# Kernel tuning notes

Measured on AMD Instinct MI355X. Metric: run time of the kernel, lower is better.

## Reference

```python
import jax, jax.numpy as jnp
import numpy as np

B, S, E, R = 128, 16, 512, 1000
_SCALE = np.float32(1.0 / np.sqrt(E))


def setup_inputs() -> dict:
    key = jax.random.key(0)
    ks = jax.random.split(key, 12)
    s = 1.0 / np.sqrt(E)
    u = lambda k, shape: jax.random.uniform(k, shape, jnp.float32, -s, s)
    emb = jax.random.normal(ks[0], (R + 1, E), jnp.float32).at[R].set(0.0)  # padding_idx row = 0
    return {
        "tokens": jax.random.randint(ks[11], (B, S), 0, R),
        "emb": emb,
        "W_ih": u(ks[1], (3 * E, E)), "W_hh": u(ks[2], (3 * E, E)),
        "b_ih": u(ks[3], (3 * E,)), "b_hh": u(ks[4], (3 * E,)),
        "w_fc": u(ks[5], (E,)), "b_fc": u(ks[6], ()),
        "Wq": u(ks[7], (E, E)), "bq": u(ks[8], (E,)),
        "Wk": u(ks[9], (E, E)), "bk": u(ks[10], (E,)),
    }


def _gru_step(x, h, W_ih, W_hh, b_ih, b_hh):
    # torch GRU cell: gates stacked as [r; z; n]
    gi = x @ W_ih.T + b_ih
    gh = h @ W_hh.T + b_hh
    ir, iz, inn = jnp.split(gi, 3, axis=-1)
    hr, hz, hn = jnp.split(gh, 3, axis=-1)
    r = jax.nn.sigmoid(ir + hr)
    z = jax.nn.sigmoid(iz + hz)
    n = jnp.tanh(inn + r * hn)
    return (1.0 - z) * n + z * h


def _attention(x, emb, Wq, bq, Wk, bk):
    # x: [B,1,E]; key = fc_k(cat(relation_emb, x)); scores = q k^T / sqrt(E)
    Bn = x.shape[0]
    rel = jnp.broadcast_to(emb[:R][None], (Bn, R, E))
    all_emb = jnp.concatenate([rel, x], axis=1)        # [B,R+1,E]
    q = x @ Wq.T + bq
    k = all_emb @ Wk.T + bk
    scores = jnp.einsum('bqe,bke->bqk', q, k) * _SCALE  # [B,1,R+1]
    return scores, all_emb


def _entropy(scores):
    lp = jax.nn.log_softmax(scores, axis=-1)
    return -jnp.sum(jnp.exp(lp) * lp, axis=-1)          # [B,1]


def _reduce(x, emb, W_ih, W_hh, b_ih, b_hh, w_fc, b_fc, Wq, bq, Wk, bk):
    Bn, L, Ed = x.shape
    if L > 2:
        # vectorized 2-step GRU over all adjacent pairs (replaces python while loop)
        h1 = _gru_step(x[:, :-1], jnp.zeros_like(x[:, :-1]), W_ih, W_hh, b_ih, b_hh)
        pairs = _gru_step(x[:, 1:], h1, W_ih, W_hh, b_ih, b_hh)   # [B,L-1,E]
        score = jax.nn.sigmoid(pairs @ w_fc + b_fc)               # [B,L-1]
        sel = jnp.argmax(score, axis=-1)                          # [B]
        barange = jnp.arange(Bn)
        pair = pairs[barange, sel][:, None]                       # [B,1,E]
        scores, all_emb = _attention(pair, emb, Wq, bq, Wk, bk)
        loss = _entropy(scores)
        prob = jax.nn.softmax(scores, axis=-1)                    # weightedAverage mask is all-False for seq_len=1
        merged = jnp.einsum('bqk,bke->bqe', prob, all_emb)[:, 0]  # [B,E]
        # output = inputs.detach().clone(); overwrite sel with merged; delete row sel+1
        out = jax.lax.stop_gradient(x).at[barange, sel].set(merged)
        j = jnp.arange(L - 1)[None]
        src = j + (j >= (sel + 1)[:, None])                       # skip zeroed row sel+1
        out = out[barange[:, None], src]                          # [B,L-1,E]
        return out, loss
    else:
        h1 = _gru_step(x[:, 0], jnp.zeros_like(x[:, 0]), W_ih, W_hh, b_ih, b_hh)
        h2 = _gru_step(x[:, 1], h1, W_ih, W_hh, b_ih, b_hh)
        return h2[:, None], jnp.zeros((Bn, 1), x.dtype)


def reference(tokens, emb, W_ih, W_hh, b_ih, b_hh, w_fc, b_fc, Wq, bq, Wk, bk):
    x = emb[tokens]                                               # [B,S,E]
    losses = []
    for _ in range(tokens.shape[1] - 1):
        x, l = _reduce(x, emb, W_ih, W_hh, b_ih, b_hh, w_fc, b_fc, Wq, bq, Wk, bk)
        losses.append(l)
    scores, _ = _attention(x, emb, Wq, bq, Wk, bk)                # x is [B,1,E]
    losses.append(_entropy(scores))
    return scores[:, 0], jnp.concatenate(losses, axis=-1)         # ([B,R+1], [B,S])
```

## Files before the change

### kernel.cpp

```cpp
#include <hip/hip_runtime.h>

#define B 128
#define S 16
#define E 512
#define R 1000
#define K3 1536
#define NW0 1920
#define NWS 256
#define NS (B * (R + 1))
#define SCALE 0.04419417382415922f

static __device__ __forceinline__ float sigm(float x) { return 1.f / (1.f + expf(-x)); }

static __device__ __forceinline__ float brsum(float v, float* sb) {
  int tid = threadIdx.x;
  sb[tid] = v; __syncthreads();
  for (int s = 128; s > 0; s >>= 1) {
    if (tid < s) sb[tid] += sb[tid + s];
    __syncthreads();
  }
  float r = sb[0]; __syncthreads();
  return r;
}
static __device__ __forceinline__ float brmax(float v, float* sb) {
  int tid = threadIdx.x;
  sb[tid] = v; __syncthreads();
  for (int s = 128; s > 0; s >>= 1) {
    if (tid < s) sb[tid] = fmaxf(sb[tid], sb[tid + s]);
    __syncthreads();
  }
  float r = sb[0]; __syncthreads();
  return r;
}
static __device__ __forceinline__ void brsum2(float v1, float v2, float* sb, float* sb2,
                                              float* o1, float* o2) {
  int tid = threadIdx.x;
  sb[tid] = v1; sb2[tid] = v2; __syncthreads();
  for (int s = 128; s > 0; s >>= 1) {
    if (tid < s) { sb[tid] += sb[tid + s]; sb2[tid] += sb2[tid + s]; }
    __syncthreads();
  }
  *o1 = sb[0]; *o2 = sb2[0]; __syncthreads();
}

#define TILE_FMA \
  _Pragma("unroll") \
  for (int k = 0; k < 16; ++k) { \
    float4 a4 = *(const float4*)&As[k][ty * 4]; \
    float4 w4 = *(const float4*)&Ws[k][tx * 4]; \
    acc[0][0] = fmaf(a4.x, w4.x, acc[0][0]); acc[0][1] = fmaf(a4.x, w4.y, acc[0][1]); \
    acc[0][2] = fmaf(a4.x, w4.z, acc[0][2]); acc[0][3] = fmaf(a4.x, w4.w, acc[0][3]); \
    acc[1][0] = fmaf(a4.y, w4.x, acc[1][0]); acc[1][1] = fmaf(a4.y, w4.y, acc[1][1]); \
    acc[1][2] = fmaf(a4.y, w4.z, acc[1][2]); acc[1][3] = fmaf(a4.y, w4.w, acc[1][3]); \
    acc[2][0] = fmaf(a4.z, w4.x, acc[2][0]); acc[2][1] = fmaf(a4.z, w4.y, acc[2][1]); \
    acc[2][2] = fmaf(a4.z, w4.z, acc[2][2]); acc[2][3] = fmaf(a4.z, w4.w, acc[2][3]); \
    acc[3][0] = fmaf(a4.w, w4.x, acc[3][0]); acc[3][1] = fmaf(a4.w, w4.y, acc[3][1]); \
    acc[3][2] = fmaf(a4.w, w4.z, acc[3][2]); acc[3][3] = fmaf(a4.w, w4.w, acc[3][3]); \
  }

#define TILE_FMA32 \
  _Pragma("unroll") \
  for (int k = 0; k < 16; ++k) { \
    float2 a2 = *(const float2*)&As[k][ty * 2]; \
    float4 w4 = *(const float4*)&Ws[k][tx * 4]; \
    acc[0][0] = fmaf(a2.x, w4.x, acc[0][0]); acc[0][1] = fmaf(a2.x, w4.y, acc[0][1]); \
    acc[0][2] = fmaf(a2.x, w4.z, acc[0][2]); acc[0][3] = fmaf(a2.x, w4.w, acc[0][3]); \
    acc[1][0] = fmaf(a2.y, w4.x, acc[1][0]); acc[1][1] = fmaf(a2.y, w4.y, acc[1][1]); \
    acc[1][2] = fmaf(a2.y, w4.z, acc[1][2]); acc[1][3] = fmaf(a2.y, w4.w, acc[1][3]); \
  }

__global__ __launch_bounds__(256) void k_gemm(const float* __restrict__ A, int lda, int M,
                                              const float* __restrict__ W, int N, int K,
                                              const float* __restrict__ bias, float scale,
                                              float* __restrict__ C, int ldc) {
  __shared__ float As[16][64];
  __shared__ float Ws[16][64];
  int tid = threadIdx.x;
  int mBase = blockIdx.y * 64;
  int nBase = blockIdx.x * 64;
  int tx = tid & 15, ty = tid >> 4;
  int li = tid & 63;
  int lk = (tid >> 6) * 4;
  float acc[4][4] = {{0.f,0.f,0.f,0.f},{0.f,0.f,0.f,0.f},{0.f,0.f,0.f,0.f},{0.f,0.f,0.f,0.f}};
  int m = mBase + li;
  const float* Arow = (m < M) ? (A + (size_t)m * lda) : nullptr;
  int n = nBase + li;
  const float* Wrow = (n < N) ? (W + (size_t)n * K) : nullptr;

  float4 av = Arow ? *(const float4*)(Arow + lk) : make_float4(0.f, 0.f, 0.f, 0.f);
  float4 wv = Wrow ? *(const float4*)(Wrow + lk) : make_float4(0.f, 0.f, 0.f, 0.f);

  for (int k0 = 0; k0 < K; k0 += 16) {
    As[lk + 0][li] = av.x; As[lk + 1][li] = av.y;
    As[lk + 2][li] = av.z; As[lk + 3][li] = av.w;
    Ws[lk + 0][li] = wv.x; Ws[lk + 1][li] = wv.y;
    Ws[lk + 2][li] = wv.z; Ws[lk + 3][li] = wv.w;
    __syncthreads();
    if (k0 + 16 < K) {
      av = Arow ? *(const float4*)(Arow + k0 + 16 + lk) : make_float4(0.f, 0.f, 0.f, 0.f);
      wv = Wrow ? *(const float4*)(Wrow + k0 + 16 + lk) : make_float4(0.f, 0.f, 0.f, 0.f);
    }
    TILE_FMA
    __syncthreads();
  }
#pragma unroll
  for (int r = 0; r < 4; ++r) {
    int mm = mBase + ty * 4 + r;
    if (mm >= M) continue;
#pragma unroll
    for (int c = 0; c < 4; ++c) {
      int nn = nBase + tx * 4 + c;
      if (nn >= N) continue;
      float v = acc[r][c] * scale;
      if (bias) v += bias[nn];
      C[(size_t)mm * ldc + nn] = v;
    }
  }
}

__global__ __launch_bounds__(256) void k_gemmD(const float* __restrict__ A, int lda, int M,
                                               const float* __restrict__ W1, int N1,
                                               const float* __restrict__ b1,
                                               float* __restrict__ C1, int ldc1,
                                               const float* __restrict__ W2, int N2,
                                               float* __restrict__ C2, int ldc2, int K) {
  __shared__ float As[16][64];
  __shared__ float Ws[16][64];
  int tid = threadIdx.x;
  int mBase = blockIdx.y * 64;
  int nBase = blockIdx.x * 64;
  int tx = tid & 15, ty = tid >> 4;
  int li = tid & 63;
  int lk = (tid >> 6) * 4;
  float acc[4][4] = {{0.f,0.f,0.f,0.f},{0.f,0.f,0.f,0.f},{0.f,0.f,0.f,0.f},{0.f,0.f,0.f,0.f}};
  int m = mBase + li;
  const float* Arow = (m < M) ? (A + (size_t)m * lda) : nullptr;
  int n = nBase + li;
  const float* Wrow = nullptr;
  if (n < N1) Wrow = W1 + (size_t)n * K;
  else if (n < N1 + N2) Wrow = W2 + (size_t)(n - N1) * K;

  float4 av = Arow ? *(const float4*)(Arow + lk) : make_float4(0.f, 0.f, 0.f, 0.f);
  float4 wv = Wrow ? *(const float4*)(Wrow + lk) : make_float4(0.f, 0.f, 0.f, 0.f);

  for (int k0 = 0; k0 < K; k0 += 16) {
    As[lk + 0][li] = av.x; As[lk + 1][li] = av.y;
    As[lk + 2][li] = av.z; As[lk + 3][li] = av.w;
    Ws[lk + 0][li] = wv.x; Ws[lk + 1][li] = wv.y;
    Ws[lk + 2][li] = wv.z; Ws[lk + 3][li] = wv.w;
    __syncthreads();
    if (k0 + 16 < K) {
      av = Arow ? *(const float4*)(Arow + k0 + 16 + lk) : make_float4(0.f, 0.f, 0.f, 0.f);
      wv = Wrow ? *(const float4*)(Wrow + k0 + 16 + lk) : make_float4(0.f, 0.f, 0.f, 0.f);
    }
    TILE_FMA
    __syncthreads();
  }
#pragma unroll
  for (int r = 0; r < 4; ++r) {
    int mm = mBase + ty * 4 + r;
    if (mm >= M) continue;
#pragma unroll
    for (int c = 0; c < 4; ++c) {
      int nn = nBase + tx * 4 + c;
      if (nn < N1) {
        float v = acc[r][c];
        if (b1) v += b1[nn];
        C1[(size_t)mm * ldc1 + nn] = v;
      } else if (nn < N1 + N2) {
        C2[(size_t)mm * ldc2 + (nn - N1)] = acc[r][c];
      }
    }
  }
}

static __device__ void dev_g64(float (*As)[64], float (*Ws)[64], int tid,
                               int mBase, int nBase,
                               const float* __restrict__ A, int lda, int M,
                               const float* __restrict__ W, int N, int K,
                               const float* __restrict__ bias, float scale,
                               float* __restrict__ C, int ldc) {
  int tx = tid & 15, ty = tid >> 4;
  int li = tid & 63;
  int lk = (tid >> 6) * 4;
  float acc[4][4] = {{0.f,0.f,0.f,0.f},{0.f,0.f,0.f,0.f},{0.f,0.f,0.f,0.f},{0.f,0.f,0.f,0.f}};
  int m = mBase + li;
  const float* Arow = (m < M) ? (A + (size_t)m * lda) : nullptr;
  int n = nBase + li;
  const float* Wrow = (n < N) ? (W + (size_t)n * K) : nullptr;

  float4 av = Arow ? *(const float4*)(Arow + lk) : make_float4(0.f, 0.f, 0.f, 0.f);
  float4 wv = Wrow ? *(const float4*)(Wrow + lk) : make_float4(0.f, 0.f, 0.f, 0.f);

  for (int k0 = 0; k0 < K; k0 += 16) {
    As[lk + 0][li] = av.x; As[lk + 1][li] = av.y;
    As[lk + 2][li] = av.z; As[lk + 3][li] = av.w;
    Ws[lk + 0][li] = wv.x; Ws[lk + 1][li] = wv.y;
    Ws[lk + 2][li] = wv.z; Ws[lk + 3][li] = wv.w;
    __syncthreads();
    if (k0 + 16 < K) {
      av = Arow ? *(const float4*)(Arow + k0 + 16 + lk) : make_float4(0.f, 0.f, 0.f, 0.f);
      wv = Wrow ? *(const float4*)(Wrow + k0 + 16 + lk) : make_float4(0.f, 0.f, 0.f, 0.f);
    }
    TILE_FMA
    __syncthreads();
  }
#pragma unroll
  for (int r = 0; r < 4; ++r) {
    int mm = mBase + ty * 4 + r;
    if (mm >= M) continue;
#pragma unroll
    for (int c = 0; c < 4; ++c) {
      int nn = nBase + tx * 4 + c;
      if (nn >= N) continue;
      float v = acc[r][c] * scale;
      if (bias) v += bias[nn];
      C[(size_t)mm * ldc + nn] = v;
    }
  }
}

static __device__ void dev_tr64(float (*t)[65], int tid, const float* __restrict__ src,
                                int Cc, float* __restrict__ dst, int ldd, int bx, int by) {
  int tx = tid & 15, ty = tid >> 4;
  int rb = by * 64, cb = bx * 64;
#pragma unroll
  for (int i = 0; i < 4; ++i) {
    int r = rb + ty + i * 16;
    float4 v = *(const float4*)(src + (size_t)r * Cc + cb + tx * 4);
    t[ty + i * 16][tx * 4 + 0] = v.x; t[ty + i * 16][tx * 4 + 1] = v.y;
    t[ty + i * 16][tx * 4 + 2] = v.z; t[ty + i * 16][tx * 4 + 3] = v.w;
  }
  __syncthreads();
#pragma unroll
  for (int i = 0; i < 4; ++i) {
    int c = cb + ty + i * 16;
    float4 v;
    v.x = t[tx * 4 + 0][ty + i * 16]; v.y = t[tx * 4 + 1][ty + i * 16];
    v.z = t[tx * 4 + 2][ty + i * 16]; v.w = t[tx * 4 + 3][ty + i * 16];
    *(float4*)(dst + (size_t)c * ldd + rb + tx * 4) = v;
  }
}

__global__ __launch_bounds__(256) void k_prep(const float* __restrict__ Wq,
                                              const float* __restrict__ Wk,
                                              const float* __restrict__ Wih,
                                              float* __restrict__ WqT,
                                              float* __restrict__ WkT,
                                              float* __restrict__ Wbig,
                                              int* __restrict__ pos,
                                              int* __restrict__ wlb,
                                              int* __restrict__ wlL,
                                              int* __restrict__ wlR,
                                              float* __restrict__ outp) {
  __shared__ float t[64][65];
  int blk = blockIdx.x, tid = threadIdx.x;
  if (blk < 64) {
    dev_tr64(t, tid, Wq, E, WqT, E, blk & 7, blk >> 3);
  } else if (blk < 128) {
    int j = blk - 64;
    dev_tr64(t, tid, Wk, E, WkT, E, j & 7, j >> 3);
  } else if (blk < 320) {
    int j = blk - 128;
    dev_tr64(t, tid, Wih, E, Wbig + (size_t)1024 * K3, K3, j & 7, j >> 3);
  } else if (blk < 328) {
    int idx = (blk - 320) * 256 + tid;
    if (idx < B * 16) pos[idx] = idx & 15;
    if (idx < NW0) {
      wlb[idx] = idx / 15;
      int i = idx % 15;
      wlL[idx] = i;
      wlR[idx] = i + 1;
    }
    if (idx < B) outp[NS + idx * 16 + 14] = 0.f;
  } else {
    int idx = (blk - 328) * 256 + tid;
    for (int i = idx; i < 24 * K3; i += 8 * 256) Wbig[(size_t)1000 * K3 + i] = 0.f;
  }
}

__global__ __launch_bounds__(256) void k_setup3(const float* __restrict__ KREL,
                                                const float* __restrict__ WqT,
                                                const float* __restrict__ WkT,
                                                const float* __restrict__ bq,
                                                const float* __restrict__ bk,
                                                float* __restrict__ Gbig,
                                                float* __restrict__ v12,
                                                float* __restrict__ c0s,
                                                float* __restrict__ gb,
                                                const int* __restrict__ tokens,
                                                const float* __restrict__ Wbig,
                                                const float* __restrict__ bih,
                                                const float* __restrict__ bhh,
                                                float* __restrict__ GI,
                                                float* __restrict__ H1P,
                                                float* __restrict__ SCT) {
  __shared__ float As[16][64];
  __shared__ float Ws[16][64];
  int blk = blockIdx.x, tid = threadIdx.x;
  if (blk < 128) {
    dev_g64(As, Ws, tid, (blk >> 3) * 64, (blk & 7) * 64, KREL, E, R, WqT, E, E,
            nullptr, 1.f, Gbig, E);
  } else if (blk < 192) {
    int j = blk - 128;
    dev_g64(As, Ws, tid, (j >> 3) * 64, (j & 7) * 64, WqT, E, E, WkT, E, E,
            nullptr, 1.f, Gbig + (size_t)1000 * E, E);
  } else if (blk < 199) {
    int m = blk - 192;
    if (m < 2) {
      int i = m * 256 + tid;
      const float* wq = WqT + (size_t)i * E;
      const float* wk = WkT + (size_t)i * E;
      float s = 0.f;
      for (int e = 0; e < E; ++e) s += wq[e] * bk[e] + bq[e] * wk[e];
      v12[i] = s;
    } else if (m == 2) {
      float* sb = (float*)As;
      float p = 0.f;
      for (int e = tid; e < E; e += 256) p += bq[e] * bk[e];
      float s = brsum(p, sb);
      if (tid == 0) c0s[0] = s;
    } else {
      int r = (m - 3) * 256 + tid;
      if (r < R) {
        const float* kr = KREL + (size_t)r * E;
        float s = 0.f;
        for (int e = 0; e < E; ++e) s += bq[e] * kr[e];
        gb[r] = s;
      }
    }
  } else if (blk < 199 + B * S) {
    int row = blk - 199;
    int tok = tokens[row];
    const float4* src = (const float4*)(Wbig + (size_t)tok * K3);
    const float4* bv = (const float4*)bih;
    float* girow = GI + (size_t)row * K3;
    float4* dst = (float4*)girow;
    for (int i = tid; i < K3 / 4; i += 256) {
      float4 a = src[i], b = bv[i];
      dst[i] = make_float4(a.x + b.x, a.y + b.y, a.z + b.z, a.w + b.w);
    }
    __syncthreads();
    float* h = H1P + (size_t)row * E;
    for (int e = tid; e < E; e += 256) {
      float r = sigm(girow[e] + bhh[e]);
      float z = sigm(girow[E + e] + bhh[E + e]);
      h[e] = (1.f - z) * tanhf(girow[2 * E + e] + r * bhh[2 * E + e]);
    }
  } else {
    int rb = blk - (199 + B * S);
    for (int m = rb * 16; m < rb * 16 + 16; ++m) {
      float* r = SCT + (size_t)m * K3;
      for (int n = tid; n < 1512; n += 256) r[n] = 0.f;
    }
  }
}

__global__ __launch_bounds__(256) void k_h1c(const int* __restrict__ xdst,
                                             const float* __restrict__ GI,
                                             const float* __restrict__ bhh,
                                             float* __restrict__ H1P) {
  int p = xdst[blockIdx.x], tid = threadIdx.x;
  const float* gi = GI + (size_t)p * K3;
  float* h = H1P + (size_t)p * E;
  for (int e = tid; e < E; e += 256) {
    float r = sigm(gi[e] + bhh[e]);
    float z = sigm(gi[E + e] + bhh[E + e]);
    h[e] = (1.f - z) * tanhf(gi[2 * E + e] + r * bhh[2 * E + e]);
  }
}

__global__ __launch_bounds__(256) void k_ghcs(const int* __restrict__ xdst,
                                              const float* __restrict__ H1P,
                                              const float* __restrict__ Whh,
                                              float* __restrict__ GHCP) {
  __shared__ float As[16][32];
  __shared__ float Ws[16][64];
  __shared__ int sp[32];
  int tid = threadIdx.x;
  int nBase = blockIdx.x * 64;
  int mBase = blockIdx.y * 32;
  int kbeg = blockIdx.z * 256;
  if (tid < 32) sp[tid] = xdst[mBase + tid];
  __syncthreads();
  int tx = tid & 15, ty = tid >> 4;
  int ar = tid & 31, ak = (tid >> 5) * 2;
  int li = tid & 63, lk = (tid >> 6) * 4;
  float acc[2][4] = {{0.f,0.f,0.f,0.f},{0.f,0.f,0.f,0.f}};
  const float* Arow = H1P + (size_t)sp[ar] * E + kbeg;
  const float* Wrow = Whh + (size_t)(nBase + li) * E + kbeg;
  float2 av = *(const float2*)(Arow + ak);
  float4 wv = *(const float4*)(Wrow + lk);
  for (int k0 = 0; k0 < 256; k0 += 16) {
    As[ak + 0][ar] = av.x; As[ak + 1][ar] = av.y;
    Ws[lk + 0][li] = wv.x; Ws[lk + 1][li] = wv.y;
    Ws[lk + 2][li] = wv.z; Ws[lk + 3][li] = wv.w;
    __syncthreads();
    if (k0 + 16 < 256) {
      av = *(const float2*)(Arow + k0 + 16 + ak);
      wv = *(const float4*)(Wrow + k0 + 16 + lk);
    }
    TILE_FMA32
    __syncthreads();
  }
#pragma unroll
  for (int r = 0; r < 2; ++r) {
    size_t crow = (size_t)sp[ty * 2 + r] * K3;
#pragma unroll
    for (int c = 0; c < 4; ++c) {
      int nn = nBase + tx * 4 + c;
      atomicAdd(&GHCP[crow + nn], acc[r][c]);
    }
  }
}

__global__ __launch_bounds__(256) void k_pairc(const int* __restrict__ wlb,
                                               const int* __restrict__ wlL,
                                               const int* __restrict__ wlR,
                                               const float* __restrict__ GI,
                                               const float* __restrict__ GHCP,
                                               const float* __restrict__ H1P,
                                               const float* __restrict__ wfc,
                                               const float* __restrict__ bfc,
                                               float* __restrict__ PAIR,
                                               float* __restrict__ SCR) {
  __shared__ float sb[256];
  int w = blockIdx.x, tid = threadIdx.x;
  int b = wlb[w], ls = wlL[w], rs = wlR[w];
  int lp = b * 16 + ls;
  const float* gr = GI + (size_t)(b * 16 + rs) * K3;
  const float* gh = GHCP + (size_t)lp * K3;
  const float* h = H1P + (size_t)lp * E;
  float* p = PAIR + (size_t)lp * E;
  float part = 0.f;
  for (int e = tid; e < E; e += 256) {
    float r = sigm(gr[e] + gh[e]);
    float z = sigm(gr[E + e] + gh[E + e]);
    float n = tanhf(gr[2 * E + e] + r * gh[2 * E + e]);
    float pv = (1.f - z) * n + z * h[e];
    p[e] = pv;
    part += pv * wfc[e];
  }
  float d = brsum(part, sb);
  if (tid == 0) SCR[b * 16 + ls] = sigm(d + bfc[0]);
}

__global__ __launch_bounds__(256) void k_qscsel(const float* __restrict__ PAIR,
                                                const float* __restrict__ SCR,
                                                const int* __restrict__ pin,
                                                int* __restrict__ pout,
                                                int* __restrict__ wlb,
                                                int* __restrict__ wlL,
                                                int* __restrict__ wlR,
                                                int* __restrict__ xdst,
                                                const float* __restrict__ Gbig,
                                                float* __restrict__ SCT,
                                                float* __restrict__ GI,
                                                const float* __restrict__ bih,
                                                float* __restrict__ GHCP,
                                                const float* __restrict__ bhh,
                                                int P, int finalMode) {
  __shared__ float As[16][32];
  __shared__ float Ws[16][64];
  __shared__ int sxd[32];
  int tid = threadIdx.x;
  int nBase = blockIdx.x * 64;
  int mBase = blockIdx.y * 32;
  int kbeg = blockIdx.z * 256;
  if (tid < 32) {
    int b = mBase + tid;
    if (finalMode) {
      int xr = b * 16 + pin[b * 16];
      sxd[tid] = xr;
      if (blockIdx.x == 0 && blockIdx.z == 0) xdst[b] = xr;
    } else {
      int L = P + 1;
      int lp[16];
      for (int i = 0; i < L; ++i) lp[i] = pin[b * 16 + i];
      float best = -1e30f; int sel = 0;
      for (int i = 0; i < P; ++i) {
        float v = SCR[b * 16 + lp[i]];
        if (v > best) { best = v; sel = i; }
      }
      int r1i = (sel + 2 < L) ? sel + 2 : L - 1;
      int l1 = lp[sel], r1 = lp[r1i];
      int l0 = (sel > 0) ? lp[sel - 1] : l1;
      int r0 = (sel > 0) ? lp[sel] : r1;
      sxd[tid] = b * 16 + l1;
      if (blockIdx.x == 0 && blockIdx.z == 0) {
        wlb[2 * b] = b;     wlL[2 * b] = l0;     wlR[2 * b] = r0;
        wlb[2 * b + 1] = b; wlL[2 * b + 1] = l1; wlR[2 * b + 1] = r1;
        xdst[b] = b * 16 + l1;
        for (int i = 0; i < L - 1; ++i)
          pout[b * 16 + i] = (i <= sel) ? lp[i] : lp[i + 1];
      }
    }
  }
  __syncthreads();
  if (!finalMode && blockIdx.z == 1) {
    if (blockIdx.x < 16) {
#pragma unroll
      for (int r = 0; r < 2; ++r) {
        float* g = GI + (size_t)sxd[blockIdx.x * 2 + r] * K3;
        for (int i = tid; i < K3; i += 256) g[i] = bih[i];
      }
    } else {
#pragma unroll
      for (int r = 0; r < 4; ++r) {
        float* g = GHCP + (size_t)sxd[(blockIdx.x - 16) * 4 + r] * K3;
        for (int i = tid; i < K3; i += 256) g[i] = bhh[i];
      }
    }
  }
  int tx = tid & 15, ty = tid >> 4;
  int ar = tid & 31, ak = (tid >> 5) * 2;
  int li = tid & 63, lk = (tid >> 6) * 4;
  float acc[2][4] = {{0.f,0.f,0.f,0.f},{0.f,0.f,0.f,0.f}};
  const float* Arow = PAIR + (size_t)sxd[ar] * E + kbeg;
  int n = nBase + li;
  const float* Wrow = (n < 1512) ? (Gbig + (size_t)n * E + kbeg) : nullptr;
  float2 av = *(const float2*)(Arow + ak);
  float4 wv = Wrow ? *(const float4*)(Wrow + lk) : make_float4(0.f, 0.f, 0.f, 0.f);
  for (int k0 = 0; k0 < 256; k0 += 16) {
    As[ak + 0][ar] = av.x; As[ak + 1][ar] = av.y;
    Ws[lk + 0][li] = wv.x; Ws[lk + 1][li] = wv.y;
    Ws[lk + 2][li] = wv.z; Ws[lk + 3][li] = wv.w;
    __syncthreads();
    if (k0 + 16 < 256) {
      av = *(const float2*)(Arow + k0 + 16 + ak);
      wv = Wrow ? *(const float4*)(Wrow + k0 + 16 + lk) : make_float4(0.f, 0.f, 0.f, 0.f);
    }
    TILE_FMA32
    __syncthreads();
  }
#pragma unroll
  for (int r = 0; r < 2; ++r) {
    int mm = mBase + ty * 2 + r;
#pragma unroll
    for (int c = 0; c < 4; ++c) {
      int nn = nBase + tx * 4 + c;
      if (nn < 1512) atomicAdd(&SCT[(size_t)mm * K3 + nn], acc[r][c]);
    }
  }
}

__global__ __launch_bounds__(256) void k_sm(float* __restrict__ SCT,
                                            const float* __restrict__ PAIR,
                                            const int* __restrict__ xdst,
                                            const float* __restrict__ v12,
                                            const float* __restrict__ c0s,
                                            float* __restrict__ outp,
                                            float* __restrict__ A2,
                                            const float* __restrict__ gb,
                                            int t, int finalMode) {
  __shared__ float sb[256];
  __shared__ float sb2[256];
  __shared__ float sps[E];
  int b = blockIdx.x, tid = threadIdx.x;
  float* row = SCT + (size_t)b * K3;
  int xr = xdst[b];
  const float* sp = PAIR + (size_t)xr * E;
  for (int i = tid; i < E; i += 256) sps[i] = sp[i];
  __syncthreads();
  float part = 0.f;
  for (int i = tid; i < E; i += 256) part += sps[i] * (row[1000 + i] + v12[i]);
  float last = (brsum(part, sb) + c0s[0]) * SCALE;
  float s[4];
  float ml = last;
#pragma unroll
  for (int q = 0; q < 4; ++q) {
    int j = tid + q * 256;
    s[q] = (j < 1000) ? (row[j] + gb[j]) * SCALE : -1e30f;
    ml = fmaxf(ml, s[q]);
  }
  float mx = brmax(ml, sb);
  float zp = 0.f, s1p = 0.f;
#pragma unroll
  for (int q = 0; q < 4; ++q) {
    int j = tid + q * 256;
    if (j < 1000) { float e = expf(s[q] - mx); zp += e; s1p += e * s[q]; }
  }
  if (tid == 0) { float e = expf(last - mx); zp += e; s1p += e * last; }
  float z, s1;
  brsum2(zp, s1p, sb, sb2, &z, &s1);
  if (tid == 0) outp[NS + b * 16 + t] = mx + logf(z) - s1 / z;
  if (!finalMode) {
    float inv = 1.f / z;
    float* a = A2 + (size_t)b * K3;
#pragma unroll
    for (int q = 0; q < 4; ++q) {
      int j = tid + q * 256;
      if (j < 1000) a[j] = expf(s[q] - mx) * inv;
    }
    if (tid < 24) a[1000 + tid] = 0.f;
    float pr = expf(last - mx) * inv;
    for (int i = tid; i < E; i += 256) a[1024 + i] = pr * sps[i];
    for (int n2 = tid; n2 < 1512; n2 += 256) row[n2] = 0.f;
  } else {
    float* so = outp + (size_t)b * (R + 1);
#pragma unroll
    for (int q = 0; q < 4; ++q) {
      int j = tid + q * 256;
      if (j < 1000) so[j] = s[q];
    }
    if (tid == 0) so[R] = last;
  }
}

__global__ __launch_bounds__(256) void k_giup(const float* __restrict__ A2,
                                              const float* __restrict__ Wbig,
                                              float* __restrict__ GI,
                                              const int* __restrict__ xdst) {
  __shared__ float As[16][32];
  __shared__ float Ws[16][64];
  int tid = threadIdx.x;
  int nBase = blockIdx.x * 64;
  int mBase = blockIdx.y * 32;
  int kbeg = blockIdx.z * 384;
  int kend = kbeg + 384;
  int tx = tid & 15, ty = tid >> 4;
  int ar = tid & 31, ak = (tid >> 5) * 2;
  int li = tid & 63, wr = tid >> 6;
  float acc[2][4] = {{0.f,0.f,0.f,0.f},{0.f,0.f,0.f,0.f}};
  const float* Arow = A2 + (size_t)(mBase + ar) * K3;
  float2 av = *(const float2*)(Arow + kbeg + ak);
  float w0 = Wbig[(size_t)(kbeg + wr * 4 + 0) * K3 + nBase + li];
  float w1 = Wbig[(size_t)(kbeg + wr * 4 + 1) * K3 + nBase + li];
  float w2 = Wbig[(size_t)(kbeg + wr * 4 + 2) * K3 + nBase + li];
  float w3 = Wbig[(size_t)(kbeg + wr * 4 + 3) * K3 + nBase + li];
  for (int k0 = kbeg; k0 < kend; k0 += 16) {
    As[ak + 0][ar] = av.x; As[ak + 1][ar] = av.y;
    Ws[wr * 4 + 0][li] = w0; Ws[wr * 4 + 1][li] = w1;
    Ws[wr * 4 + 2][li] = w2; Ws[wr * 4 + 3][li] = w3;
    __syncthreads();
    if (k0 + 16 < kend) {
      av = *(const float2*)(Arow + k0 + 16 + ak);
      w0 = Wbig[(size_t)(k0 + 16 + wr * 4 + 0) * K3 + nBase + li];
      w1 = Wbig[(size_t)(k0 + 16 + wr * 4 + 1) * K3 + nBase + li];
      w2 = Wbig[(size_t)(k0 + 16 + wr * 4 + 2) * K3 + nBase + li];
      w3 = Wbig[(size_t)(k0 + 16 + wr * 4 + 3) * K3 + nBase + li];
    }
    TILE_FMA32
    __syncthreads();
  }
#pragma unroll
  for (int r = 0; r < 2; ++r) {
    int mm = mBase + ty * 2 + r;
    size_t crow = (size_t)xdst[mm] * K3;
#pragma unroll
    for (int c = 0; c < 4; ++c) {
      int nn = nBase + tx * 4 + c;
      atomicAdd(&GI[crow + nn], acc[r][c]);
    }
  }
}

extern "C" void kernel_launch(void* const* d_in, const int* in_sizes, int n_in,
                              void* d_out, int out_size, void* d_ws, size_t ws_size,
                              hipStream_t stream) {
  (void)in_sizes; (void)n_in; (void)out_size; (void)ws_size;
  const int* tokens = (const int*)d_in[0];
  const float* emb = (const float*)d_in[1];
  const float* W_ih = (const float*)d_in[2];
  const float* W_hh = (const float*)d_in[3];
  const float* b_ih = (const float*)d_in[4];
  const float* b_hh = (const float*)d_in[5];
  const float* w_fc = (const float*)d_in[6];
  const float* b_fc = (const float*)d_in[7];
  const float* Wq = (const float*)d_in[8];
  const float* bq = (const float*)d_in[9];
  const float* Wk = (const float*)d_in[10];
  const float* bk = (const float*)d_in[11];
  float* out = (float*)d_out;

  float* ws = (float*)d_ws;
  size_t o = 0;
  float* GI = ws + o;    o += (size_t)B * S * K3;
  float* GHCP = ws + o;  o += (size_t)B * S * K3;
  float* H1P = ws + o;   o += (size_t)B * S * E;
  float* PAIR = ws + o;  o += (size_t)B * S * E;
  float* Wbig = ws + o;  o += (size_t)K3 * K3;
  float* Gbig = ws + o;  o += (size_t)1512 * E;
  float* KREL = ws + o;  o += (size_t)R * E;
  float* WqT = ws + o;   o += (size_t)E * E;
  float* WkT = ws + o;   o += (size_t)E * E;
  float* SCT = ws + o;   o += (size_t)B * K3;
  float* A2 = ws + o;    o += (size_t)B * K3;
  float* gb = ws + o;    o += 1024;
  float* v12 = ws + o;   o += 512;
  float* c0s = ws + o;   o += 16;
  float* SCR = ws + o;   o += B * 16;
  int* pos0 = (int*)(ws + o); o += B * 16;
  int* pos1 = (int*)(ws + o); o += B * 16;
  int* wlb = (int*)(ws + o);  o += NW0;
  int* wlL = (int*)(ws + o);  o += NW0;
  int* wlR = (int*)(ws + o);  o += NW0;
  int* xdst = (int*)(ws + o); o += B;

  k_prep<<<336, 256, 0, stream>>>(Wq, Wk, W_ih, WqT, WkT, Wbig, pos0, wlb, wlL, wlR, out);
  k_gemmD<<<dim3(32, 16), 256, 0, stream>>>(emb, E, R, Wk, E, bk, KREL, E,
                                            W_ih, K3, Wbig, K3, E);
  k_setup3<<<199 + B * S + 8, 256, 0, stream>>>(KREL, WqT, WkT, bq, bk, Gbig, v12, c0s,
                                                gb, tokens, Wbig, b_ih, b_hh, GI, H1P, SCT);
  k_gemm<<<dim3(24, 32), 256, 0, stream>>>(H1P, E, B * S, W_hh, K3, E, b_hh, 1.f,
                                           GHCP, K3);
  k_pairc<<<NW0, 256, 0, stream>>>(wlb, wlL, wlR, GI, GHCP, H1P, w_fc, b_fc, PAIR, SCR);

  for (int t = 0; t < 14; ++t) {
    int* pin = (t & 1) ? pos1 : pos0;
    int* pout = (t & 1) ? pos0 : pos1;
    k_qscsel<<<dim3(24, 4, 2), 256, 0, stream>>>(PAIR, SCR, pin, pout, wlb, wlL, wlR,
                                                 xdst, Gbig, SCT, GI, b_ih, GHCP, b_hh,
                                                 15 - t, 0);
    k_sm<<<B, 256, 0, stream>>>(SCT, PAIR, xdst, v12, c0s, out, A2, gb, t, 0);
    k_giup<<<dim3(24, 4, 4), 256, 0, stream>>>(A2, Wbig, GI, xdst);
    k_h1c<<<B, 256, 0, stream>>>(xdst, GI, b_hh, H1P);
    k_ghcs<<<dim3(24, 4, 2), 256, 0, stream>>>(xdst, H1P, W_hh, GHCP);
    k_pairc<<<NWS, 256, 0, stream>>>(wlb, wlL, wlR, GI, GHCP, H1P, w_fc, b_fc, PAIR, SCR);
  }

  k_qscsel<<<dim3(24, 4, 2), 256, 0, stream>>>(PAIR, SCR, pos0, pos1, wlb, wlL, wlR,
                                               xdst, Gbig, SCT, GI, b_ih, GHCP, b_hh,
                                               1, 1);
  k_sm<<<B, 256, 0, stream>>>(SCT, PAIR, xdst, v12, c0s, out, A2, gb, 15, 1);
}
```

Measured before the change: 1.337 ms.

## Precompute first GRU step per vocabulary row and refactor attention key algebra

Measured after the change: 1.326 ms. Within noise of the previous version (-0.9%).

```diff
diff --git a/kernel.cpp b/kernel.cpp
--- a/kernel.cpp
+++ b/kernel.cpp
@@ -174,52 +174,6 @@
   }
 }
 
-static __device__ void dev_g64(float (*As)[64], float (*Ws)[64], int tid,
-                               int mBase, int nBase,
-                               const float* __restrict__ A, int lda, int M,
-                               const float* __restrict__ W, int N, int K,
-                               const float* __restrict__ bias, float scale,
-                               float* __restrict__ C, int ldc) {
-  int tx = tid & 15, ty = tid >> 4;
-  int li = tid & 63;
-  int lk = (tid >> 6) * 4;
-  float acc[4][4] = {{0.f,0.f,0.f,0.f},{0.f,0.f,0.f,0.f},{0.f,0.f,0.f,0.f},{0.f,0.f,0.f,0.f}};
-  int m = mBase + li;
-  const float* Arow = (m < M) ? (A + (size_t)m * lda) : nullptr;
-  int n = nBase + li;
-  const float* Wrow = (n < N) ? (W + (size_t)n * K) : nullptr;
-
-  float4 av = Arow ? *(const float4*)(Arow + lk) : make_float4(0.f, 0.f, 0.f, 0.f);
-  float4 wv = Wrow ? *(const float4*)(Wrow + lk) : make_float4(0.f, 0.f, 0.f, 0.f);
-
-  for (int k0 = 0; k0 < K; k0 += 16) {
-    As[lk + 0][li] = av.x; As[lk + 1][li] = av.y;
-    As[lk + 2][li] = av.z; As[lk + 3][li] = av.w;
-    Ws[lk + 0][li] = wv.x; Ws[lk + 1][li] = wv.y;
-    Ws[lk + 2][li] = wv.z; Ws[lk + 3][li] = wv.w;
-    __syncthreads();
-    if (k0 + 16 < K) {
-      av = Arow ? *(const float4*)(Arow + k0 + 16 + lk) : make_float4(0.f, 0.f, 0.f, 0.f);
-      wv = Wrow ? *(const float4*)(Wrow + k0 + 16 + lk) : make_float4(0.f, 0.f, 0.f, 0.f);
-    }
-    TILE_FMA
-    __syncthreads();
-  }
-#pragma unroll
-  for (int r = 0; r < 4; ++r) {
-    int mm = mBase + ty * 4 + r;
-    if (mm >= M) continue;
-#pragma unroll
-    for (int c = 0; c < 4; ++c) {
-      int nn = nBase + tx * 4 + c;
-      if (nn >= N) continue;
-      float v = acc[r][c] * scale;
-      if (bias) v += bias[nn];
-      C[(size_t)mm * ldc + nn] = v;
-    }
-  }
-}
-
 static __device__ void dev_tr64(float (*t)[65], int tid, const float* __restrict__ src,
                                 int Cc, float* __restrict__ dst, int ldd, int bx, int by) {
   int tx = tid & 15, ty = tid >> 4;
@@ -245,26 +199,25 @@
 __global__ __launch_bounds__(256) void k_prep(const float* __restrict__ Wq,
                                               const float* __restrict__ Wk,
                                               const float* __restrict__ Wih,
-                                              float* __restrict__ WqT,
-                                              float* __restrict__ WkT,
                                               float* __restrict__ Wbig,
                                               int* __restrict__ pos,
                                               int* __restrict__ wlb,
                                               int* __restrict__ wlL,
                                               int* __restrict__ wlR,
-                                              float* __restrict__ outp) {
+                                              float* __restrict__ outp,
+                                              float* __restrict__ Gbig,
+                                              const float* __restrict__ bq,
+                                              const float* __restrict__ bk,
+                                              float* __restrict__ v12,
+                                              float* __restrict__ bw,
+                                              float* __restrict__ wv3,
+                                              float* __restrict__ c0s) {
   __shared__ float t[64][65];
   int blk = blockIdx.x, tid = threadIdx.x;
-  if (blk < 64) {
-    dev_tr64(t, tid, Wq, E, WqT, E, blk & 7, blk >> 3);
-  } else if (blk < 128) {
-    int j = blk - 64;
-    dev_tr64(t, tid, Wk, E, WkT, E, j & 7, j >> 3);
-  } else if (blk < 320) {
-    int j = blk - 128;
-    dev_tr64(t, tid, Wih, E, Wbig + (size_t)1024 * K3, K3, j & 7, j >> 3);
-  } else if (blk < 328) {
-    int idx = (blk - 320) * 256 + tid;
+  if (blk < 192) {
+    dev_tr64(t, tid, Wih, E, Wbig + (size_t)1024 * K3, K3, blk & 7, blk >> 3);
+  } else if (blk < 200) {
+    int idx = (blk - 192) * 256 + tid;
     if (idx < B * 16) pos[idx] = idx & 15;
     if (idx < NW0) {
       wlb[idx] = idx / 15;
@@ -273,87 +226,156 @@
       wlR[idx] = i + 1;
     }
     if (idx < B) outp[NS + idx * 16 + 14] = 0.f;
+  } else if (blk < 208) {
+    int idx = (blk - 200) * 256 + tid;
+    for (int i = idx; i < 24 * K3; i += 8 * 256) Wbig[(size_t)1000 * K3 + i] = 0.f;
+  } else if (blk < 272) {
+    int j = blk - 208;
+    int fT = (j & 7) * 64, iT = (j >> 3) * 64;
+    float (*As)[64] = (float(*)[64])&t[0][0];
+    float (*Ws)[64] = (float(*)[64])&t[20][0];
+    int tx = tid & 15, ty = tid >> 4;
+    int li = tid & 63, lk = (tid >> 6) * 4;
+    float acc[4][4] = {{0.f,0.f,0.f,0.f},{0.f,0.f,0.f,0.f},{0.f,0.f,0.f,0.f},{0.f,0.f,0.f,0.f}};
+    float a0 = Wq[(size_t)(lk + 0) * E + iT + li];
+    float a1 = Wq[(size_t)(lk + 1) * E + iT + li];
+    float a2 = Wq[(size_t)(lk + 2) * E + iT + li];
+    float a3 = Wq[(size_t)(lk + 3) * E + iT + li];
+    float w0 = Wk[(size_t)(lk + 0) * E + fT + li];
+    float w1 = Wk[(size_t)(lk + 1) * E + fT + li];
+    float w2 = Wk[(size_t)(lk + 2) * E + fT + li];
+    float w3 = Wk[(size_t)(lk + 3) * E + fT + li];
+    for (int e0 = 0; e0 < E; e0 += 16) {
+      As[lk + 0][li] = a0; As[lk + 1][li] = a1;
+      As[lk + 2][li] = a2; As[lk + 3][li] = a3;
+      Ws[lk + 0][li] = w0; Ws[lk + 1][li] = w1;
+      Ws[lk + 2][li] = w2; Ws[lk + 3][li] = w3;
+      __syncthreads();
+      if (e0 + 16 < E) {
+        a0 = Wq[(size_t)(e0 + 16 + lk + 0) * E + iT + li];
+        a1 = Wq[(size_t)(e0 + 16 + lk + 1) * E + iT + li];
+        a2 = Wq[(size_t)(e0 + 16 + lk + 2) * E + iT + li];
+        a3 = Wq[(size_t)(e0 + 16 + lk + 3) * E + iT + li];
+        w0 = Wk[(size_t)(e0 + 16 + lk + 0) * E + fT + li];
+        w1 = Wk[(size_t)(e0 + 16 + lk + 1) * E + fT + li];
+        w2 = Wk[(size_t)(e0 + 16 + lk + 2) * E + fT + li];
+        w3 = Wk[(size_t)(e0 + 16 + lk + 3) * E + fT + li];
+      }
+      TILE_FMA
+      __syncthreads();
+    }
+#pragma unroll
+    for (int r = 0; r < 4; ++r)
+#pragma unroll
+      for (int c = 0; c < 4; ++c)
+        Gbig[(size_t)(1000 + iT + ty * 4 + r) * E + fT + tx * 4 + c] = acc[r][c];
+  } else if (blk < 274) {
+    int i = (blk - 272) * 256 + tid;
+    float s = 0.f;
+    for (int e = 0; e < E; ++e) s += Wq[(size_t)e * E + i] * bk[e] + bq[e] * Wk[(size_t)e * E + i];
+    v12[i] = s;
+  } else if (blk < 276) {
+    int i = (blk - 274) * 256 + tid;
+    float s = 0.f;
+    for (int e = 0; e < E; ++e) s += bk[e] * Wq[(size_t)e * E + i];
+    bw[i] = s;
+  } else if (blk < 278) {
+    int f = (blk - 276) * 256 + tid;
+    float s = 0.f;
+    for (int e = 0; e < E; ++e) s += bq[e] * Wk[(size_t)e * E + f];
+    wv3[f] = s;
   } else {
-    int idx = (blk - 328) * 256 + tid;
-    for (int i = idx; i < 24 * K3; i += 8 * 256) Wbig[(size_t)1000 * K3 + i] = 0.f;
-  }
-}
-
-__global__ __launch_bounds__(256) void k_setup3(const float* __restrict__ KREL,
-                                                const float* __restrict__ WqT,
-                                                const float* __restrict__ WkT,
-                                                const float* __restrict__ bq,
-                                                const float* __restrict__ bk,
-                                                float* __restrict__ Gbig,
-                                                float* __restrict__ v12,
-                                                float* __restrict__ c0s,
-                                                float* __restrict__ gb,
-                                                const int* __restrict__ tokens,
+    float* sb = &t[0][0];
+    float p = 0.f;
+    for (int e = tid; e < E; e += 256) p += bq[e] * bk[e];
+    float s = brsum(p, sb);
+    if (tid == 0) c0s[0] = s;
+  }
+}
+
+__global__ __launch_bounds__(256) void k_setupB(const int* __restrict__ tokens,
                                                 const float* __restrict__ Wbig,
                                                 const float* __restrict__ bih,
                                                 const float* __restrict__ bhh,
+                                                const float* __restrict__ emb,
+                                                const float* __restrict__ wv3,
                                                 float* __restrict__ GI,
-                                                float* __restrict__ H1P,
-                                                float* __restrict__ SCT) {
-  __shared__ float As[16][64];
-  __shared__ float Ws[16][64];
+                                                float* __restrict__ H1V,
+                                                float* __restrict__ SCT,
+                                                float* __restrict__ gb) {
   int blk = blockIdx.x, tid = threadIdx.x;
-  if (blk < 128) {
-    dev_g64(As, Ws, tid, (blk >> 3) * 64, (blk & 7) * 64, KREL, E, R, WqT, E, E,
-            nullptr, 1.f, Gbig, E);
-  } else if (blk < 192) {
-    int j = blk - 128;
-    dev_g64(As, Ws, tid, (j >> 3) * 64, (j & 7) * 64, WqT, E, E, WkT, E, E,
-            nullptr, 1.f, Gbig + (size_t)1000 * E, E);
-  } else if (blk < 199) {
-    int m = blk - 192;
-    if (m < 2) {
-      int i = m * 256 + tid;
-      const float* wq = WqT + (size_t)i * E;
-      const float* wk = WkT + (size_t)i * E;
-      float s = 0.f;
-      for (int e = 0; e < E; ++e) s += wq[e] * bk[e] + bq[e] * wk[e];
-      v12[i] = s;
-    } else if (m == 2) {
-      float* sb = (float*)As;
-      float p = 0.f;
-      for (int e = tid; e < E; e += 256) p += bq[e] * bk[e];
-      float s = brsum(p, sb);
-      if (tid == 0) c0s[0] = s;
-    } else {
-      int r = (m - 3) * 256 + tid;
-      if (r < R) {
-        const float* kr = KREL + (size_t)r * E;
-        float s = 0.f;
-        for (int e = 0; e < E; ++e) s += bq[e] * kr[e];
-        gb[r] = s;
-      }
-    }
-  } else if (blk < 199 + B * S) {
-    int row = blk - 199;
-    int tok = tokens[row];
+  if (blk < 1000) {
+    const float* ew = Wbig + (size_t)blk * K3;
+    float* h = H1V + (size_t)blk * E;
+    for (int e = tid; e < E; e += 256) {
+      float g0 = ew[e] + bih[e];
+      float g1 = ew[E + e] + bih[E + e];
+      float g2 = ew[2 * E + e] + bih[2 * E + e];
+      float r = sigm(g0 + bhh[e]);
+      float z = sigm(g1 + bhh[E + e]);
+      h[e] = (1.f - z) * tanhf(g2 + r * bhh[2 * E + e]);
+    }
+  } else if (blk < 1000 + B * S) {
+    int p = blk - 1000;
+    int tok = tokens[p];
     const float4* src = (const float4*)(Wbig + (size_t)tok * K3);
     const float4* bv = (const float4*)bih;
-    float* girow = GI + (size_t)row * K3;
-    float4* dst = (float4*)girow;
+    float4* dst = (float4*)(GI + (size_t)p * K3);
     for (int i = tid; i < K3 / 4; i += 256) {
       float4 a = src[i], b = bv[i];
       dst[i] = make_float4(a.x + b.x, a.y + b.y, a.z + b.z, a.w + b.w);
     }
-    __syncthreads();
-    float* h = H1P + (size_t)row * E;
-    for (int e = tid; e < E; e += 256) {
-      float r = sigm(girow[e] + bhh[e]);
-      float z = sigm(girow[E + e] + bhh[E + e]);
-      h[e] = (1.f - z) * tanhf(girow[2 * E + e] + r * bhh[2 * E + e]);
-    }
-  } else {
-    int rb = blk - (199 + B * S);
+  } else if (blk < 1000 + B * S + 8) {
+    int rb = blk - (1000 + B * S);
     for (int m = rb * 16; m < rb * 16 + 16; ++m) {
       float* r = SCT + (size_t)m * K3;
       for (int n = tid; n < 1512; n += 256) r[n] = 0.f;
     }
-  }
+  } else {
+    int r = (blk - (1000 + B * S + 8)) * 256 + tid;
+    if (r < R) {
+      const float* er = emb + (size_t)r * E;
+      float s = 0.f;
+      for (int f = 0; f < E; ++f) s += er[f] * wv3[f];
+      gb[r] = s;
+    }
+  }
+}
+
+__global__ __launch_bounds__(256) void k_pairc0(const int* __restrict__ tokens,
+                                                const float* __restrict__ GI,
+                                                const float* __restrict__ GHCV,
+                                                const float* __restrict__ H1V,
+                                                const float* __restrict__ wfc,
+                                                const float* __restrict__ bfc,
+                                                float* __restrict__ PAIR,
+                                                float* __restrict__ SCR,
+                                                float* __restrict__ H1P,
+                                                float* __restrict__ GHCP) {
+  __shared__ float sb[256];
+  int w = blockIdx.x, tid = threadIdx.x;
+  int b = w / 15, i = w % 15;
+  int lp = b * 16 + i;
+  int tok = tokens[lp];
+  const float* gr = GI + (size_t)(lp + 1) * K3;
+  const float* gh = GHCV + (size_t)tok * K3;
+  const float* h = H1V + (size_t)tok * E;
+  float* ghp = GHCP + (size_t)lp * K3;
+  float* hp = H1P + (size_t)lp * E;
+  float* p = PAIR + (size_t)lp * E;
+  float part = 0.f;
+  for (int e = tid; e < E; e += 256) {
+    float g0 = gh[e], g1 = gh[E + e], g2 = gh[2 * E + e], he = h[e];
+    ghp[e] = g0; ghp[E + e] = g1; ghp[2 * E + e] = g2; hp[e] = he;
+    float r = sigm(gr[e] + g0);
+    float z = sigm(gr[E + e] + g1);
+    float n = tanhf(gr[2 * E + e] + r * g2);
+    float pv = (1.f - z) * n + z * he;
+    p[e] = pv;
+    part += pv * wfc[e];
+  }
+  float d = brsum(part, sb);
+  if (tid == 0) SCR[lp] = sigm(d + bfc[0]);
 }
 
 __global__ __launch_bounds__(256) void k_h1c(const int* __restrict__ xdst,
@@ -548,6 +570,7 @@
                                             const float* __restrict__ PAIR,
                                             const int* __restrict__ xdst,
                                             const float* __restrict__ v12,
+                                            const float* __restrict__ bw,
                                             const float* __restrict__ c0s,
                                             float* __restrict__ outp,
                                             float* __restrict__ A2,
@@ -562,15 +585,21 @@
   const float* sp = PAIR + (size_t)xr * E;
   for (int i = tid; i < E; i += 256) sps[i] = sp[i];
   __syncthreads();
-  float part = 0.f;
-  for (int i = tid; i < E; i += 256) part += sps[i] * (row[1000 + i] + v12[i]);
-  float last = (brsum(part, sb) + c0s[0]) * SCALE;
+  float part = 0.f, pbw = 0.f;
+  for (int i = tid; i < E; i += 256) {
+    part += sps[i] * (row[1000 + i] + v12[i]);
+    pbw += sps[i] * bw[i];
+  }
+  float ps, pb;
+  brsum2(part, pbw, sb, sb2, &ps, &pb);
+  float last = (ps + c0s[0]) * SCALE;
+  float shift = pb + c0s[0];
   float s[4];
   float ml = last;
 #pragma unroll
   for (int q = 0; q < 4; ++q) {
     int j = tid + q * 256;
-    s[q] = (j < 1000) ? (row[j] + gb[j]) * SCALE : -1e30f;
+    s[q] = (j < 1000) ? (row[j] + gb[j] + shift) * SCALE : -1e30f;
     ml = fmaxf(ml, s[q]);
   }
   float mx = brmax(ml, sb);
@@ -681,13 +710,14 @@
   float* PAIR = ws + o;  o += (size_t)B * S * E;
   float* Wbig = ws + o;  o += (size_t)K3 * K3;
   float* Gbig = ws + o;  o += (size_t)1512 * E;
-  float* KREL = ws + o;  o += (size_t)R * E;
-  float* WqT = ws + o;   o += (size_t)E * E;
-  float* WkT = ws + o;   o += (size_t)E * E;
+  float* H1V = ws + o;   o += (size_t)1024 * E;
+  float* GHCV = ws + o;  o += (size_t)1024 * K3;
   float* SCT = ws + o;   o += (size_t)B * K3;
   float* A2 = ws + o;    o += (size_t)B * K3;
   float* gb = ws + o;    o += 1024;
   float* v12 = ws + o;   o += 512;
+  float* bw = ws + o;    o += 512;
+  float* wv3 = ws + o;   o += 512;
   float* c0s = ws + o;   o += 16;
   float* SCR = ws + o;   o += B * 16;
   int* pos0 = (int*)(ws + o); o += B * 16;
@@ -697,14 +727,16 @@
   int* wlR = (int*)(ws + o);  o += NW0;
   int* xdst = (int*)(ws + o); o += B;
 
-  k_prep<<<336, 256, 0, stream>>>(Wq, Wk, W_ih, WqT, WkT, Wbig, pos0, wlb, wlL, wlR, out);
-  k_gemmD<<<dim3(32, 16), 256, 0, stream>>>(emb, E, R, Wk, E, bk, KREL, E,
-                                            W_ih, K3, Wbig, K3, E);
-  k_setup3<<<199 + B * S + 8, 256, 0, stream>>>(KREL, WqT, WkT, bq, bk, Gbig, v12, c0s,
-                                                gb, tokens, Wbig, b_ih, b_hh, GI, H1P, SCT);
-  k_gemm<<<dim3(24, 32), 256, 0, stream>>>(H1P, E, B * S, W_hh, K3, E, b_hh, 1.f,
-                                           GHCP, K3);
-  k_pairc<<<NW0, 256, 0, stream>>>(wlb, wlL, wlR, GI, GHCP, H1P, w_fc, b_fc, PAIR, SCR);
+  k_prep<<<279, 256, 0, stream>>>(Wq, Wk, W_ih, Wbig, pos0, wlb, wlL, wlR, out,
+                                  Gbig, bq, bk, v12, bw, wv3, c0s);
+  k_gemmD<<<dim3(32, 16), 256, 0, stream>>>(emb, E, R, W_ih, K3, nullptr, Wbig, K3,
+                                            Gbig + (size_t)1000 * E, 512, Gbig, E, E);
+  k_setupB<<<1000 + B * S + 8 + 4, 256, 0, stream>>>(tokens, Wbig, b_ih, b_hh, emb,
+                                                     wv3, GI, H1V, SCT, gb);
+  k_gemm<<<dim3(24, 16), 256, 0, stream>>>(H1V, E, 1000, W_hh, K3, E, b_hh, 1.f,
+                                           GHCV, K3);
+  k_pairc0<<<NW0, 256, 0, stream>>>(tokens, GI, GHCV, H1V, w_fc, b_fc, PAIR, SCR,
+                                    H1P, GHCP);
 
   for (int t = 0; t < 14; ++t) {
     int* pin = (t & 1) ? pos1 : pos0;
@@ -712,7 +744,7 @@
     k_qscsel<<<dim3(24, 4, 2), 256, 0, stream>>>(PAIR, SCR, pin, pout, wlb, wlL, wlR,
                                                  xdst, Gbig, SCT, GI, b_ih, GHCP, b_hh,
                                                  15 - t, 0);
-    k_sm<<<B, 256, 0, stream>>>(SCT, PAIR, xdst, v12, c0s, out, A2, gb, t, 0);
+    k_sm<<<B, 256, 0, stream>>>(SCT, PAIR, xdst, v12, bw, c0s, out, A2, gb, t, 0);
     k_giup<<<dim3(24, 4, 4), 256, 0, stream>>>(A2, Wbig, GI, xdst);
     k_h1c<<<B, 256, 0, stream>>>(xdst, GI, b_hh, H1P);
     k_ghcs<<<dim3(24, 4, 2), 256, 0, stream>>>(xdst, H1P, W_hh, GHCP);
@@ -722,5 +754,5 @@
   k_qscsel<<<dim3(24, 4, 2), 256, 0, stream>>>(PAIR, SCR, pos0, pos1, wlb, wlL, wlR,
                                                xdst, Gbig, SCT, GI, b_ih, GHCP, b_hh,
                                                1, 1);
-  k_sm<<<B, 256, 0, stream>>>(SCT, PAIR, xdst, v12, c0s, out, A2, gb, 15, 1);
-}
+  k_sm<<<B, 256, 0, stream>>>(SCT, PAIR, xdst, v12, bw, c0s, out, A2, gb, 15, 1);
+}
```
